# Kernel tuning notes

Measured on AMD Instinct MI355X. Metric: run time of the kernel, lower is better.

## Reference

```python
import jax, jax.numpy as jnp
import numpy as np
from jax import lax

N_LAYER = 4
D_MODEL = 512
N_HEAD = 8
D_HEAD = 64
D_INNER = 2048
KERNEL = 9
POOL = 8
N_CLASSES = 10
BATCH = 4
RAW_LEN = 8192


def setup_inputs() -> dict:
    key = jax.random.key(0)
    ks = jax.random.split(key, 12)
    s = 0.02
    return {
        "signal": jax.random.normal(ks[0], (BATCH, RAW_LEN), jnp.float32),
        "conv_w": jax.random.normal(ks[1], (KERNEL, 1, D_MODEL), jnp.float32) * s,
        "conv_b": jnp.zeros((D_MODEL,), jnp.float32),
        "qkv_w": jax.random.normal(ks[2], (N_LAYER, D_MODEL, 3 * N_HEAD * D_HEAD), jnp.float32) * s,
        "r_w": jax.random.normal(ks[3], (N_LAYER, D_MODEL, N_HEAD * D_HEAD), jnp.float32) * s,
        "o_w": jax.random.normal(ks[4], (N_LAYER, N_HEAD * D_HEAD, D_MODEL), jnp.float32) * s,
        "ff1_w": jax.random.normal(ks[5], (N_LAYER, D_MODEL, D_INNER), jnp.float32) * s,
        "ff1_b": jnp.zeros((N_LAYER, D_INNER), jnp.float32),
        "ff2_w": jax.random.normal(ks[6], (N_LAYER, D_INNER, D_MODEL), jnp.float32) * s,
        "ff2_b": jnp.zeros((N_LAYER, D_MODEL), jnp.float32),
        "r_w_bias": jax.random.normal(ks[7], (N_HEAD, D_HEAD), jnp.float32) * s,
        "r_r_bias": jax.random.normal(ks[8], (N_HEAD, D_HEAD), jnp.float32) * s,
        "fc_w": jax.random.normal(ks[9], (D_MODEL, N_CLASSES), jnp.float32) * s,
        "fc_b": jnp.zeros((N_CLASSES,), jnp.float32),
    }


def _rel_shift(x):
    # x: [qlen, rlen, bsz, n_head]; TF-XL pad/reshape/slice trick
    q, r, b, n = x.shape
    x = jnp.pad(x, ((0, 0), (1, 0), (0, 0), (0, 0)))
    x = x.reshape(r + 1, q, b, n)[1:]
    return x.reshape(q, r, b, n)


def _forward(signal, conv_w, conv_b, qkv_w, r_w, o_w, ff1_w, ff1_b, ff2_w,
             ff2_b, r_w_bias, r_r_bias, fc_w, fc_b):
    # Conv1D (valid) -> ReLU -> AveragePooling1D
    x = signal[:, :, None]  # [B, L, 1]
    x = lax.conv_general_dilated(x, conv_w, (1,), 'VALID',
                                 dimension_numbers=('NWC', 'WIO', 'NWC')) + conv_b
    x = jax.nn.relu(x)
    B, Lp, D = x.shape
    S = Lp // POOL  # Lp is divisible by POOL for our sizes (keras valid pooling)
    x = x[:, :S * POOL].reshape(B, S, POOL, D).mean(axis=2)
    core = x.transpose(1, 0, 2)  # [S, B, D]

    # sinusoidal relative positional embedding, pos_seq = S-1 .. -(S-1)
    pos_seq = jnp.arange(S - 1, -S, -1, dtype=core.dtype)  # [2S-1]
    inv_freq = 1.0 / (10000.0 ** (jnp.arange(0, D, 2, dtype=core.dtype) / D))
    sin_inp = pos_seq[:, None] * inv_freq[None, :]
    pos_emb = jnp.concatenate([jnp.sin(sin_inp), jnp.cos(sin_inp)], -1)  # [2S-1, D]

    scale = 1.0 / np.sqrt(D_HEAD).astype(np.float32)
    for l in range(N_LAYER):
        heads = core @ qkv_w[l]  # [S, B, 3*H*Dh]
        q, k, v = jnp.split(heads, 3, axis=-1)
        q = q.reshape(S, B, N_HEAD, D_HEAD)
        k = k.reshape(S, B, N_HEAD, D_HEAD)
        v = v.reshape(S, B, N_HEAD, D_HEAD)
        rk = (pos_emb @ r_w[l]).reshape(2 * S - 1, N_HEAD, D_HEAD)

        AC = jnp.einsum('ibnd,jbnd->ijbn', q + r_w_bias, k)      # content term
        BD = jnp.einsum('ibnd,jnd->ijbn', q + r_r_bias, rk)      # position term
        BD = _rel_shift(BD)[:, :S]                                # [S, S, B, H]
        attn_prob = jax.nn.softmax((AC + BD) * scale, axis=1)
        attn_vec = jnp.einsum('ijbn,jbnd->ibnd', attn_prob, v)
        attn_out = attn_vec.reshape(S, B, N_HEAD * D_HEAD) @ o_w[l]
        core = core + attn_out

        # position-wise FF with residual
        h = jax.nn.relu(core @ ff1_w[l] + ff1_b[l]) @ ff2_w[l] + ff2_b[l]
        core = core + h

    # classification head on last timestep
    return core[-1] @ fc_w + fc_b  # [B, n_classes]


def reference(signal, conv_w, conv_b, qkv_w, r_w, o_w, ff1_w, ff1_b, ff2_w,
              ff2_b, r_w_bias, r_r_bias, fc_w, fc_b):
    return _forward(signal, conv_w, conv_b, qkv_w, r_w, o_w, ff1_w, ff1_b,
                    ff2_w, ff2_b, r_w_bias, r_r_bias, fc_w, fc_b)
```

## Files before the change

kernel.cpp:

```cpp
#include <hip/hip_runtime.h>
#include <math.h>

#define S_LEN   1023
#define BATCH_N 4
#define DMODEL  512
#define NHEAD   8
#define DHEAD   64
#define DINNER  2048
#define NLAYER  4
#define RAWLEN  8192
#define POOLW   8
#define KERNW   9
#define RLEN    (2*S_LEN-1)
#define MROWS   (S_LEN*BATCH_N)

using bf16x8 = __attribute__((ext_vector_type(8))) short;
using f32x4  = __attribute__((ext_vector_type(4))) float;

__device__ __forceinline__ unsigned short f2bf(float f) {
    union { float f; unsigned int u; } v; v.f = f;
    unsigned int u = v.u;
    return (unsigned short)((u + 0x7fffu + ((u >> 16) & 1u)) >> 16);
}
__device__ __forceinline__ float bf2f(unsigned short h) {
    union { unsigned int u; float f; } v; v.u = ((unsigned int)h) << 16;
    return v.f;
}

__device__ __forceinline__ void gload_lds16(const void* g, void* l) {
    using gvoid = const __attribute__((address_space(1))) void;
    using lvoid = __attribute__((address_space(3))) void;
    gvoid* gp = reinterpret_cast<gvoid*>(reinterpret_cast<unsigned long long>(g));
    lvoid* lp = reinterpret_cast<lvoid*>((unsigned int)reinterpret_cast<unsigned long long>(l));
    __builtin_amdgcn_global_load_lds(gp, lp, 16, 0, 0);
}

__global__ __launch_bounds__(512) void conv_pool_kernel(
    const float* __restrict__ sig, const float* __restrict__ cw,
    const float* __restrict__ cb, float* __restrict__ core,
    unsigned short* __restrict__ core_bf)
{
    int s = blockIdx.x, b = blockIdx.y, d = threadIdx.x;
    __shared__ float sseg[POOLW + KERNW - 1];
    if (d < POOLW + KERNW - 1) sseg[d] = sig[b*RAWLEN + s*POOLW + d];
    __syncthreads();
    float w[KERNW];
#pragma unroll
    for (int k = 0; k < KERNW; k++) w[k] = cw[k*DMODEL + d];
    float bias = cb[d];
    float acc = 0.f;
#pragma unroll
    for (int p = 0; p < POOLW; p++) {
        float c = bias;
#pragma unroll
        for (int k = 0; k < KERNW; k++) c = fmaf(sseg[p+k], w[k], c);
        acc += fmaxf(c, 0.f);
    }
    float v = acc * (1.0f/POOLW);
    core[(s*BATCH_N + b)*DMODEL + d] = v;
    core_bf[(s*BATCH_N + b)*DMODEL + d] = f2bf(v);
}

__global__ __launch_bounds__(512) void posemb_kernel(unsigned short* __restrict__ pe)
{
    int j = blockIdx.x, d = threadIdx.x;
    float pos = (float)(S_LEN - 1 - j);
    int i = (d < 256) ? d : d - 256;
    float invf = exp2f(-(float)i * (13.287712f/256.0f));
    float a = pos * invf;
    pe[j*DMODEL + d] = f2bf((d < 256) ? __sinf(a) : __cosf(a));
}

__global__ __launch_bounds__(256) void transpose_all_kernel(
    const float* __restrict__ qw, const float* __restrict__ rw,
    const float* __restrict__ ow, const float* __restrict__ f1,
    const float* __restrict__ f2,
    unsigned short* __restrict__ qT, unsigned short* __restrict__ rT,
    unsigned short* __restrict__ oT, unsigned short* __restrict__ f1T,
    unsigned short* __restrict__ f2T)
{
    int id = blockIdx.x;
    const float* W; unsigned short* Wt; int K, N, bx, by;
    if (id < 768)       { W = qw;  Wt = qT;  K = 512;  N = 1536; bx = id % 48; by = id / 48; }
    else if (id < 1024) { id -= 768;  W = rw;  Wt = rT;  K = 512;  N = 512;  bx = id % 16; by = id / 16; }
    else if (id < 1280) { id -= 1024; W = ow;  Wt = oT;  K = 512;  N = 512;  bx = id % 16; by = id / 16; }
    else if (id < 2304) { id -= 1280; W = f1;  Wt = f1T; K = 512;  N = 2048; bx = id % 64; by = id / 64; }
    else                { id -= 2304; W = f2;  Wt = f2T; K = 2048; N = 512;  bx = id % 16; by = id / 16; }

    __shared__ float L[32][33];
    int n0 = bx*32, k0 = by*32;
    int t = threadIdx.x;
    int kk = t>>3, nq = (t&7)*4;
    float4 v = *reinterpret_cast<const float4*>(&W[(size_t)(k0+kk)*N + n0 + nq]);
    L[kk][nq+0]=v.x; L[kk][nq+1]=v.y; L[kk][nq+2]=v.z; L[kk][nq+3]=v.w;
    __syncthreads();
    int nn = t>>3, kq = (t&7)*4;
    ushort4 o;
    o.x = f2bf(L[kq+0][nn]); o.y = f2bf(L[kq+1][nn]);
    o.z = f2bf(L[kq+2][nn]); o.w = f2bf(L[kq+3][nn]);
    *reinterpret_cast<ushort4*>(&Wt[(size_t)(n0+nn)*K + k0 + kq]) = o;
}

__global__ __launch_bounds__(256) void vtrans_kernel(
    const unsigned short* __restrict__ heads, unsigned short* __restrict__ vt)
{
    int j0 = blockIdx.x * 64;
    int bn = blockIdx.y; int b = bn >> 3, n = bn & 7;
    __shared__ unsigned short Ls[64*68];
    int t = threadIdx.x;
#pragma unroll
    for (int p = 0; p < 2; p++) {
        int jr = (t>>3) + p*32, sl = (t&7)*8;
        int gj = j0 + jr; if (gj > S_LEN-1) gj = S_LEN-1;
        const unsigned short* src = heads + (size_t)(gj*BATCH_N + b)*1536 + 1024 + n*64 + sl;
        ushort4 a = *reinterpret_cast<const ushort4*>(src);
        ushort4 c = *reinterpret_cast<const ushort4*>(src+4);
        *reinterpret_cast<ushort4*>(&Ls[jr*68 + sl])   = a;
        *reinterpret_cast<ushort4*>(&Ls[jr*68 + sl+4]) = c;
    }
    __syncthreads();
#pragma unroll
    for (int p = 0; p < 2; p++) {
        int d = (t>>3) + p*32, jq = (t&7)*8;
        ushort4 o0, o1;
        o0.x = Ls[(jq+0)*68 + d]; o0.y = Ls[(jq+1)*68 + d];
        o0.z = Ls[(jq+2)*68 + d]; o0.w = Ls[(jq+3)*68 + d];
        o1.x = Ls[(jq+4)*68 + d]; o1.y = Ls[(jq+5)*68 + d];
        o1.z = Ls[(jq+6)*68 + d]; o1.w = Ls[(jq+7)*68 + d];
        unsigned short* dst = vt + ((size_t)bn*64 + d)*1024 + j0 + jq;
        *reinterpret_cast<ushort4*>(dst) = o0;
        *reinterpret_cast<ushort4*>(dst+4) = o1;
    }
}

template<int BN, bool ACCUM, bool BIAS, bool RELU, bool WF32, bool WBF>
__device__ __forceinline__ void gemm_body(
    const unsigned short* __restrict__ A, const unsigned short* __restrict__ Bt,
    const float* __restrict__ bias, float* __restrict__ C,
    unsigned short* __restrict__ Cb, int M, int N, int K, int bm, int bn,
    unsigned short* As, unsigned short* Bs)
{
    constexpr int MF = (BN == 128) ? 4 : 2;
    int tid = threadIdx.x, lane = tid & 63, wid = tid >> 6;

    f32x4 acc[MF][4];
#pragma unroll
    for (int m=0;m<MF;m++)
#pragma unroll
        for (int n=0;n<4;n++) acc[m][n] = (f32x4){0.f,0.f,0.f,0.f};

    int r0 = wid*16 + (lane>>2);
    int slot = (lane&3)*8;
    int ga0 = bm + r0;      if (ga0 > M-1) ga0 = M-1;
    int ga1 = bm + r0 + 64; if (ga1 > M-1) ga1 = M-1;
    const unsigned short* pA0 = A  + (size_t)ga0*K + slot;
    const unsigned short* pA1 = A  + (size_t)ga1*K + slot;
    const unsigned short* pB0 = Bt + (size_t)(bn + r0)*K + slot;
    const unsigned short* pB1 = (BN==128) ? Bt + (size_t)(bn + r0 + 64)*K + slot : nullptr;
    char* lA0 = (char*)As + wid*1024;
    char* lA1 = (char*)As + (wid+4)*1024;
    char* lB0 = (char*)Bs + wid*1024;
    char* lB1 = (char*)Bs + (wid+4)*1024;

    int ar = (BN==128 ? (wid>>1)*64 : wid*32) + (lane&15);
    int br = (BN==128 ? (wid&1)*64 : 0) + (lane&15);
    int kc = (lane>>4)*8;

    for (int k0 = 0; k0 < K; k0 += 32) {
        __syncthreads();
        gload_lds16(pA0, lA0);
        gload_lds16(pA1, lA1);
        gload_lds16(pB0, lB0);
        if (BN == 128) gload_lds16(pB1, lB1);
        pA0 += 32; pA1 += 32; pB0 += 32; if (BN==128) pB1 += 32;
        __syncthreads();
        bf16x8 a[MF], b[4];
#pragma unroll
        for (int m=0;m<MF;m++) a[m] = *reinterpret_cast<const bf16x8*>(&As[(ar + m*16)*32 + kc]);
#pragma unroll
        for (int n=0;n<4;n++) b[n] = *reinterpret_cast<const bf16x8*>(&Bs[(br + n*16)*32 + kc]);
#pragma unroll
        for (int m=0;m<MF;m++)
#pragma unroll
            for (int n=0;n<4;n++)
                acc[m][n] = __builtin_amdgcn_mfma_f32_16x16x32_bf16(a[m], b[n], acc[m][n], 0,0,0);
    }

    int col0 = bn + (BN==128 ? (wid&1)*64 : 0) + (lane&15);
    int rbase = bm + (BN==128 ? (wid>>1)*64 : wid*32) + (lane>>4)*4;
#pragma unroll
    for (int m=0;m<MF;m++) {
#pragma unroll
        for (int n=0;n<4;n++) {
            int col = col0 + n*16;
            float bv = BIAS ? bias[col] : 0.f;
#pragma unroll
            for (int r=0;r<4;r++) {
                int row = rbase + m*16 + r;
                if (row < M) {
                    float v = acc[m][n][r] + bv;
                    if (RELU) v = fmaxf(v, 0.f);
                    size_t off = (size_t)row*N + col;
                    if (ACCUM) v += C[off];
                    if (WF32) C[off] = v;
                    if (WBF)  Cb[off] = f2bf(v);
                }
            }
        }
    }
}

template<int BN, bool ACCUM, bool BIAS, bool RELU, bool WF32, bool WBF>
__global__ __launch_bounds__(256) void gemm_mfma(
    const unsigned short* __restrict__ A, const unsigned short* __restrict__ Bt,
    const float* __restrict__ bias, float* __restrict__ C,
    unsigned short* __restrict__ Cb, int M, int N, int K)
{
    __shared__ unsigned short As[128*32];
    __shared__ unsigned short Bs[BN*32];
    gemm_body<BN,ACCUM,BIAS,RELU,WF32,WBF>(A, Bt, bias, C, Cb, M, N, K,
        blockIdx.y*128, blockIdx.x*BN, As, Bs);
}

__global__ __launch_bounds__(256) void gemm_qkvrk_kernel(
    const unsigned short* __restrict__ core_bf, const unsigned short* __restrict__ qkvT,
    unsigned short* __restrict__ heads,
    const unsigned short* __restrict__ pe_bf, const unsigned short* __restrict__ rwT,
    unsigned short* __restrict__ rk_bf)
{
    __shared__ unsigned short As[128*32];
    __shared__ unsigned short Bs[64*32];
    if (blockIdx.x < 24) {
        gemm_body<64,false,false,false,false,true>(core_bf, qkvT, nullptr, nullptr, heads,
            MROWS, 3*DMODEL, DMODEL, blockIdx.y*128, blockIdx.x*64, As, Bs);
    } else {
        if (blockIdx.y >= 16) return;
        gemm_body<64,false,false,false,false,true>(pe_bf, rwT, nullptr, nullptr, rk_bf,
            RLEN, DMODEL, DMODEL, blockIdx.y*128, (blockIdx.x-24)*64, As, Bs);
    }
}

template<bool ACCUM, bool BIAS, bool RELU, bool WF32, bool WBF>
__global__ __launch_bounds__(256) void gemm_mfma64(
    const unsigned short* __restrict__ A, const unsigned short* __restrict__ Bt,
    const float* __restrict__ bias, float* __restrict__ C,
    unsigned short* __restrict__ Cb, int M, int N, int K)
{
    __shared__ unsigned short As[64*32];
    __shared__ unsigned short Bs[64*32];
    int bm = blockIdx.y * 64, bn = blockIdx.x * 64;
    int tid = threadIdx.x, lane = tid & 63, wid = tid >> 6;
    int wr = wid >> 1, wc = wid & 1;

    f32x4 acc[2][2];
#pragma unroll
    for (int m=0;m<2;m++)
#pragma unroll
        for (int n=0;n<2;n++) acc[m][n] = (f32x4){0.f,0.f,0.f,0.f};

    int r0 = wid*16 + (lane>>2);
    int slot = (lane&3)*8;
    int ga = bm + r0; if (ga > M-1) ga = M-1;
    const unsigned short* pA = A  + (size_t)ga*K + slot;
    const unsigned short* pB = Bt + (size_t)(bn + r0)*K + slot;
    char* lA = (char*)As + wid*1024;
    char* lB = (char*)Bs + wid*1024;

    int ar = wr*32 + (lane&15);
    int br = wc*32 + (lane&15);
    int kc = (lane>>4)*8;

    for (int k0 = 0; k0 < K; k0 += 32) {
        __syncthreads();
        gload_lds16(pA, lA);
        gload_lds16(pB, lB);
        pA += 32; pB += 32;
        __syncthreads();
        bf16x8 a[2], b[2];
#pragma unroll
        for (int m=0;m<2;m++) a[m] = *reinterpret_cast<const bf16x8*>(&As[(ar + m*16)*32 + kc]);
#pragma unroll
        for (int n=0;n<2;n++) b[n] = *reinterpret_cast<const bf16x8*>(&Bs[(br + n*16)*32 + kc]);
#pragma unroll
        for (int m=0;m<2;m++)
#pragma unroll
            for (int n=0;n<2;n++)
                acc[m][n] = __builtin_amdgcn_mfma_f32_16x16x32_bf16(a[m], b[n], acc[m][n], 0,0,0);
    }

    int col0 = bn + wc*32 + (lane&15);
    int rbase = bm + wr*32 + (lane>>4)*4;
#pragma unroll
    for (int m=0;m<2;m++) {
#pragma unroll
        for (int n=0;n<2;n++) {
            int col = col0 + n*16;
            float bv = BIAS ? bias[col] : 0.f;
#pragma unroll
            for (int r=0;r<4;r++) {
                int row = rbase + m*16 + r;
                if (row < M) {
                    float v = acc[m][n][r] + bv;
                    if (RELU) v = fmaxf(v, 0.f);
                    size_t off = (size_t)row*N + col;
                    if (ACCUM) v += C[off];
                    if (WF32) C[off] = v;
                    if (WBF)  Cb[off] = f2bf(v);
                }
            }
        }
    }
}

#define TI 32
#define TJ 32
#define PSTR 40
#define ACSTR 36
#define BDSTR 68

__global__ __launch_bounds__(256) void attn_mfma_kernel(
    const unsigned short* __restrict__ heads,
    const unsigned short* __restrict__ rk,
    const unsigned short* __restrict__ vt,
    const float* __restrict__ rwb, const float* __restrict__ rrb,
    unsigned short* __restrict__ av)
{
    int i0 = blockIdx.x * TI;
    int bn = blockIdx.y; int b = bn >> 3, n = bn & 7;
    int tid = threadIdx.x, lane = tid & 63, wid = tid >> 6;
    int mi = wid >> 1;
    int half = wid & 1;
    int kc = (lane>>4)*8;
    int l15 = lane & 15;

    __shared__ float Sac[TI*ACSTR];
    __shared__ float Sbd[TI*BDSTR];
    __shared__ unsigned short Pb[TI*PSTR];
    __shared__ float mrow[TI], lrow[TI], frow[TI];

    const int base0 = (S_LEN-1) - i0 - (TI-1);

    bf16x8 qwf0, qwf1, qrf0, qrf1;
    {
        int gi = i0 + mi*16 + l15; if (gi > S_LEN-1) gi = S_LEN-1;
        const unsigned short* qb = heads + (size_t)(gi*BATCH_N + b)*1536 + n*64;
        bf16x8 u0 = *reinterpret_cast<const bf16x8*>(qb + kc);
        bf16x8 u1 = *reinterpret_cast<const bf16x8*>(qb + 32 + kc);
#pragma unroll
        for (int e=0;e<8;e++) {
            float f0 = bf2f((unsigned short)u0[e]);
            float f1 = bf2f((unsigned short)u1[e]);
            qwf0[e] = (short)f2bf(f0 + rwb[n*64 + kc + e]);
            qrf0[e] = (short)f2bf(f0 + rrb[n*64 + kc + e]);
            qwf1[e] = (short)f2bf(f1 + rwb[n*64 + 32 + kc + e]);
            qrf1[e] = (short)f2bf(f1 + rrb[n*64 + 32 + kc + e]);
        }
    }
    if (tid < TI) { mrow[tid] = -1e30f; lrow[tid] = 0.f; }

    f32x4 Oa[2];
    Oa[0] = (f32x4){0.f,0.f,0.f,0.f};
    Oa[1] = (f32x4){0.f,0.f,0.f,0.f};

    int rw = mi*16 + (lane>>4)*4;
    const unsigned short* vrow = vt + (size_t)bn*64*1024;

    for (int t = 0; t < 32; t++) {
        int j0 = t * TJ;
        __syncthreads();

        {
            int gj = j0 + half*16 + l15; if (gj > S_LEN-1) gj = S_LEN-1;
            const unsigned short* kb = heads + (size_t)(gj*BATCH_N + b)*1536 + 512 + n*64;
            bf16x8 kf0 = *reinterpret_cast<const bf16x8*>(kb + kc);
            bf16x8 kf1 = *reinterpret_cast<const bf16x8*>(kb + 32 + kc);
            f32x4 s = (f32x4){0.f,0.f,0.f,0.f};
            s = __builtin_amdgcn_mfma_f32_16x16x32_bf16(qwf0, kf0, s, 0,0,0);
            s = __builtin_amdgcn_mfma_f32_16x16x32_bf16(qwf1, kf1, s, 0,0,0);
            int ci = half*16 + l15;
#pragma unroll
            for (int r=0;r<4;r++) Sac[(rw+r)*ACSTR + ci] = s[r];
        }
        if (t == 0) {
#pragma unroll
            for (int nn=0;nn<2;nn++) {
                int w = (half*2+nn)*16 + l15;
                int gr = base0 + w; gr = gr < 0 ? 0 : (gr > RLEN-1 ? RLEN-1 : gr);
                const unsigned short* rb = rk + (size_t)gr*DMODEL + n*64;
                bf16x8 rf0 = *reinterpret_cast<const bf16x8*>(rb + kc);
                bf16x8 rf1 = *reinterpret_cast<const bf16x8*>(rb + 32 + kc);
                f32x4 sb = (f32x4){0.f,0.f,0.f,0.f};
                sb = __builtin_amdgcn_mfma_f32_16x16x32_bf16(qrf0, rf0, sb, 0,0,0);
                sb = __builtin_amdgcn_mfma_f32_16x16x32_bf16(qrf1, rf1, sb, 0,0,0);
#pragma unroll
                for (int r=0;r<4;r++) Sbd[(rw+r)*BDSTR + w] = sb[r];
            }
        } else {
            int pblk = ((t & 1) ? 0 : 2) + half;
            int w = pblk*16 + l15;
            int off = 32*(t+1) + (w & 31);
            int gr = base0 + off; gr = gr < 0 ? 0 : (gr > RLEN-1 ? RLEN-1 : gr);
            const unsigned short* rb = rk + (size_t)gr*DMODEL + n*64;
            bf16x8 rf0 = *reinterpret_cast<const bf16x8*>(rb + kc);
            bf16x8 rf1 = *reinterpret_cast<const bf16x8*>(rb + 32 + kc);
            f32x4 sb = (f32x4){0.f,0.f,0.f,0.f};
            sb = __builtin_amdgcn_mfma_f32_16x16x32_bf16(qrf0, rf0, sb, 0,0,0);
            sb = __builtin_amdgcn_mfma_f32_16x16x32_bf16(qrf1, rf1, sb, 0,0,0);
#pragma unroll
            for (int r=0;r<4;r++) Sbd[(rw+r)*BDSTR + w] = sb[r];
        }
        __syncthreads();

        {
            int r = tid>>3, seg = tid&7, jl = seg*4;
            float4 ac = *reinterpret_cast<const float4*>(&Sac[r*ACSTR + jl]);
            int cbase = 32*t + (TI-1) - r;
            float s0 = (ac.x + Sbd[r*BDSTR + ((cbase+jl+0)&63)]) * 0.125f;
            float s1 = (ac.y + Sbd[r*BDSTR + ((cbase+jl+1)&63)]) * 0.125f;
            float s2 = (ac.z + Sbd[r*BDSTR + ((cbase+jl+2)&63)]) * 0.125f;
            float s3 = (ac.w + Sbd[r*BDSTR + ((cbase+jl+3)&63)]) * 0.125f;
            int jg = j0 + jl;
            if (jg+0 >= S_LEN) s0 = -1e30f;
            if (jg+1 >= S_LEN) s1 = -1e30f;
            if (jg+2 >= S_LEN) s2 = -1e30f;
            if (jg+3 >= S_LEN) s3 = -1e30f;
            float tm = fmaxf(fmaxf(s0,s1), fmaxf(s2,s3));
            tm = fmaxf(tm, __shfl_xor(tm, 1));
            tm = fmaxf(tm, __shfl_xor(tm, 2));
            tm = fmaxf(tm, __shfl_xor(tm, 4));
            float mo = mrow[r];
            float mnew = fmaxf(mo, tm);
            float f = __expf(mo - mnew);
            float e0 = __expf(s0 - mnew), e1 = __expf(s1 - mnew);
            float e2 = __expf(s2 - mnew), e3 = __expf(s3 - mnew);
            float ssum = e0+e1+e2+e3;
            ssum += __shfl_xor(ssum, 1);
            ssum += __shfl_xor(ssum, 2);
            ssum += __shfl_xor(ssum, 4);
            if (seg == 0) {
                mrow[r] = mnew;
                lrow[r] = lrow[r]*f + ssum;
                frow[r] = f;
            }
            ushort4 pw;
            pw.x = f2bf(e0); pw.y = f2bf(e1); pw.z = f2bf(e2); pw.w = f2bf(e3);
            *reinterpret_cast<ushort4*>(&Pb[r*PSTR + jl]) = pw;
        }
        __syncthreads();

        {
            float f0 = frow[rw+0], f1 = frow[rw+1], f2 = frow[rw+2], f3 = frow[rw+3];
#pragma unroll
            for (int nn=0;nn<2;nn++) {
                Oa[nn][0] *= f0; Oa[nn][1] *= f1; Oa[nn][2] *= f2; Oa[nn][3] *= f3;
            }
            bf16x8 pf = *reinterpret_cast<const bf16x8*>(&Pb[(mi*16 + l15)*PSTR + kc]);
#pragma unroll
            for (int nn=0;nn<2;nn++) {
                int d = (half*2+nn)*16 + l15;
                bf16x8 vf = *reinterpret_cast<const bf16x8*>(&vrow[(size_t)d*1024 + j0 + kc]);
                Oa[nn] = __builtin_amdgcn_mfma_f32_16x16x32_bf16(pf, vf, Oa[nn], 0,0,0);
            }
        }
    }
    __syncthreads();

    {
        float linv[4];
#pragma unroll
        for (int r=0;r<4;r++) linv[r] = 1.0f / lrow[rw+r];
#pragma unroll
        for (int nn=0;nn<2;nn++) {
            int d = (half*2+nn)*16 + l15;
#pragma unroll
            for (int r=0;r<4;r++) {
                int gi = i0 + rw + r;
                if (gi < S_LEN)
                    av[(size_t)(gi*BATCH_N + b)*DMODEL + n*64 + d] = f2bf(Oa[nn][r]*linv[r]);
            }
        }
    }
}

__global__ __launch_bounds__(64) void final_kernel(
    const float* __restrict__ core, const float* __restrict__ fcw,
    const float* __restrict__ fcb, float* __restrict__ out)
{
    int idx = blockIdx.x;
    int b = idx / 10, c = idx % 10;
    int lane = threadIdx.x;
    const float* row = &core[(size_t)((S_LEN-1)*BATCH_N + b)*DMODEL];
    float acc = 0.f;
    for (int d = lane; d < DMODEL; d += 64)
        acc = fmaf(row[d], fcw[d*10 + c], acc);
#pragma unroll
    for (int off = 32; off; off >>= 1) acc += __shfl_xor(acc, off);
    if (lane == 0) out[b*10 + c] = acc + fcb[c];
}

extern "C" void kernel_launch(void* const* d_in, const int* in_sizes, int n_in,
                              void* d_out, int out_size, void* d_ws, size_t ws_size,
                              hipStream_t stream)
{
    const float* sig   = (const float*)d_in[0];
    const float* cw    = (const float*)d_in[1];
    const float* cb    = (const float*)d_in[2];
    const float* qkv_w = (const float*)d_in[3];
    const float* r_w   = (const float*)d_in[4];
    const float* o_w   = (const float*)d_in[5];
    const float* ff1_w = (const float*)d_in[6];
    const float* ff1_b = (const float*)d_in[7];
    const float* ff2_w = (const float*)d_in[8];
    const float* ff2_b = (const float*)d_in[9];
    const float* rwb   = (const float*)d_in[10];
    const float* rrb   = (const float*)d_in[11];
    const float* fcw   = (const float*)d_in[12];
    const float* fcb   = (const float*)d_in[13];
    float* out = (float*)d_out;

    float* core = (float*)d_ws;
    unsigned short* core_bf = (unsigned short*)(core + (size_t)MROWS*DMODEL);
    unsigned short* pe_bf   = core_bf + (size_t)MROWS*DMODEL;
    unsigned short* rk_bf   = pe_bf   + (size_t)RLEN*DMODEL;
    unsigned short* av_bf   = rk_bf   + (size_t)RLEN*DMODEL;
    unsigned short* big_bf  = av_bf   + (size_t)MROWS*DMODEL;
    unsigned short* qkvT = big_bf + (size_t)MROWS*DINNER;
    unsigned short* rwT  = qkvT + (size_t)(3*DMODEL)*DMODEL;
    unsigned short* owT  = rwT  + (size_t)DMODEL*DMODEL;
    unsigned short* ff1T = owT  + (size_t)DMODEL*DMODEL;
    unsigned short* ff2T = ff1T + (size_t)DINNER*DMODEL;
    unsigned short* vt   = ff2T + (size_t)DMODEL*DINNER;

    conv_pool_kernel<<<dim3(S_LEN, BATCH_N), 512, 0, stream>>>(sig, cw, cb, core, core_bf);
    posemb_kernel<<<RLEN, 512, 0, stream>>>(pe_bf);

    for (int l = 0; l < NLAYER; l++) {
        transpose_all_kernel<<<3328, 256, 0, stream>>>(
            qkv_w + (size_t)l*DMODEL*(3*DMODEL),
            r_w   + (size_t)l*DMODEL*DMODEL,
            o_w   + (size_t)l*DMODEL*DMODEL,
            ff1_w + (size_t)l*DMODEL*DINNER,
            ff2_w + (size_t)l*DINNER*DMODEL,
            qkvT, rwT, owT, ff1T, ff2T);

        gemm_qkvrk_kernel<<<dim3(32,32), 256, 0, stream>>>(
            core_bf, qkvT, big_bf, pe_bf, rwT, rk_bf);
        vtrans_kernel<<<dim3(16,32), 256, 0, stream>>>(big_bf, vt);
        attn_mfma_kernel<<<dim3(32,32), 256, 0, stream>>>(big_bf, rk_bf, vt, rwb, rrb, av_bf);
        gemm_mfma64<true,false,false,true,true><<<dim3(8,64), 256, 0, stream>>>(
            av_bf, owT, nullptr, core, core_bf, MROWS, DMODEL, DMODEL);
        gemm_mfma<128,false,true,true,false,true><<<dim3(16,32), 256, 0, stream>>>(
            core_bf, ff1T, ff1_b + (size_t)l*DINNER, nullptr, big_bf, MROWS, DINNER, DMODEL);
        gemm_mfma64<true,true,false,true,true><<<dim3(8,64), 256, 0, stream>>>(
            big_bf, ff2T, ff2_b + (size_t)l*DMODEL, core, core_bf, MROWS, DMODEL, DINNER);
    }

    final_kernel<<<40, 64, 0, stream>>>(core, fcw, fcb, out);
}
```

Before: 753.0 us.

## Drop V transpose kernel and prefetch K/R fragments across attention iterations

Removes the separate vtrans kernel and instead gathers V fragments inside the attention kernel with scalar strided 16-bit loads straight from the qkv buffer. K and positional-key fragments for the next tile are now loaded one iteration ahead into registers, so their latency overlaps the current softmax work. This saves one kernel launch and a global round trip per layer. In exchange, the V loads become uncoalesced 2-byte accesses per element, and register pressure rises.

```diff
diff --git a/kernel.cpp b/kernel.cpp
--- a/kernel.cpp
+++ b/kernel.cpp
@@ -101,38 +101,6 @@
     *reinterpret_cast<ushort4*>(&Wt[(size_t)(n0+nn)*K + k0 + kq]) = o;
 }
 
-__global__ __launch_bounds__(256) void vtrans_kernel(
-    const unsigned short* __restrict__ heads, unsigned short* __restrict__ vt)
-{
-    int j0 = blockIdx.x * 64;
-    int bn = blockIdx.y; int b = bn >> 3, n = bn & 7;
-    __shared__ unsigned short Ls[64*68];
-    int t = threadIdx.x;
-#pragma unroll
-    for (int p = 0; p < 2; p++) {
-        int jr = (t>>3) + p*32, sl = (t&7)*8;
-        int gj = j0 + jr; if (gj > S_LEN-1) gj = S_LEN-1;
-        const unsigned short* src = heads + (size_t)(gj*BATCH_N + b)*1536 + 1024 + n*64 + sl;
-        ushort4 a = *reinterpret_cast<const ushort4*>(src);
-        ushort4 c = *reinterpret_cast<const ushort4*>(src+4);
-        *reinterpret_cast<ushort4*>(&Ls[jr*68 + sl])   = a;
-        *reinterpret_cast<ushort4*>(&Ls[jr*68 + sl+4]) = c;
-    }
-    __syncthreads();
-#pragma unroll
-    for (int p = 0; p < 2; p++) {
-        int d = (t>>3) + p*32, jq = (t&7)*8;
-        ushort4 o0, o1;
-        o0.x = Ls[(jq+0)*68 + d]; o0.y = Ls[(jq+1)*68 + d];
-        o0.z = Ls[(jq+2)*68 + d]; o0.w = Ls[(jq+3)*68 + d];
-        o1.x = Ls[(jq+4)*68 + d]; o1.y = Ls[(jq+5)*68 + d];
-        o1.z = Ls[(jq+6)*68 + d]; o1.w = Ls[(jq+7)*68 + d];
-        unsigned short* dst = vt + ((size_t)bn*64 + d)*1024 + j0 + jq;
-        *reinterpret_cast<ushort4*>(dst) = o0;
-        *reinterpret_cast<ushort4*>(dst+4) = o1;
-    }
-}
-
 template<int BN, bool ACCUM, bool BIAS, bool RELU, bool WF32, bool WBF>
 __device__ __forceinline__ void gemm_body(
     const unsigned short* __restrict__ A, const unsigned short* __restrict__ Bt,
@@ -321,7 +289,6 @@
 __global__ __launch_bounds__(256) void attn_mfma_kernel(
     const unsigned short* __restrict__ heads,
     const unsigned short* __restrict__ rk,
-    const unsigned short* __restrict__ vt,
     const float* __restrict__ rwb, const float* __restrict__ rrb,
     unsigned short* __restrict__ av)
 {
@@ -363,17 +330,32 @@
     Oa[1] = (f32x4){0.f,0.f,0.f,0.f};
 
     int rw = mi*16 + (lane>>4)*4;
-    const unsigned short* vrow = vt + (size_t)bn*64*1024;
+
+    bf16x8 kf0, kf1, rA0, rA1, rB0, rB1;
+    {
+        int gj = half*16 + l15; if (gj > S_LEN-1) gj = S_LEN-1;
+        const unsigned short* kb = heads + (size_t)(gj*BATCH_N + b)*1536 + 512 + n*64;
+        kf0 = *reinterpret_cast<const bf16x8*>(kb + kc);
+        kf1 = *reinterpret_cast<const bf16x8*>(kb + 32 + kc);
+    }
+    {
+        int w = (half*2+0)*16 + l15;
+        int gr = base0 + w; gr = gr < 0 ? 0 : (gr > RLEN-1 ? RLEN-1 : gr);
+        const unsigned short* rb = rk + (size_t)gr*DMODEL + n*64;
+        rA0 = *reinterpret_cast<const bf16x8*>(rb + kc);
+        rA1 = *reinterpret_cast<const bf16x8*>(rb + 32 + kc);
+        w = (half*2+1)*16 + l15;
+        gr = base0 + w; gr = gr < 0 ? 0 : (gr > RLEN-1 ? RLEN-1 : gr);
+        rb = rk + (size_t)gr*DMODEL + n*64;
+        rB0 = *reinterpret_cast<const bf16x8*>(rb + kc);
+        rB1 = *reinterpret_cast<const bf16x8*>(rb + 32 + kc);
+    }
 
     for (int t = 0; t < 32; t++) {
         int j0 = t * TJ;
         __syncthreads();
 
         {
-            int gj = j0 + half*16 + l15; if (gj > S_LEN-1) gj = S_LEN-1;
-            const unsigned short* kb = heads + (size_t)(gj*BATCH_N + b)*1536 + 512 + n*64;
-            bf16x8 kf0 = *reinterpret_cast<const bf16x8*>(kb + kc);
-            bf16x8 kf1 = *reinterpret_cast<const bf16x8*>(kb + 32 + kc);
             f32x4 s = (f32x4){0.f,0.f,0.f,0.f};
             s = __builtin_amdgcn_mfma_f32_16x16x32_bf16(qwf0, kf0, s, 0,0,0);
             s = __builtin_amdgcn_mfma_f32_16x16x32_bf16(qwf1, kf1, s, 0,0,0);
@@ -382,32 +364,52 @@
             for (int r=0;r<4;r++) Sac[(rw+r)*ACSTR + ci] = s[r];
         }
         if (t == 0) {
-#pragma unroll
-            for (int nn=0;nn<2;nn++) {
-                int w = (half*2+nn)*16 + l15;
-                int gr = base0 + w; gr = gr < 0 ? 0 : (gr > RLEN-1 ? RLEN-1 : gr);
-                const unsigned short* rb = rk + (size_t)gr*DMODEL + n*64;
-                bf16x8 rf0 = *reinterpret_cast<const bf16x8*>(rb + kc);
-                bf16x8 rf1 = *reinterpret_cast<const bf16x8*>(rb + 32 + kc);
-                f32x4 sb = (f32x4){0.f,0.f,0.f,0.f};
-                sb = __builtin_amdgcn_mfma_f32_16x16x32_bf16(qrf0, rf0, sb, 0,0,0);
-                sb = __builtin_amdgcn_mfma_f32_16x16x32_bf16(qrf1, rf1, sb, 0,0,0);
-#pragma unroll
-                for (int r=0;r<4;r++) Sbd[(rw+r)*BDSTR + w] = sb[r];
-            }
+            f32x4 sb = (f32x4){0.f,0.f,0.f,0.f};
+            sb = __builtin_amdgcn_mfma_f32_16x16x32_bf16(qrf0, rA0, sb, 0,0,0);
+            sb = __builtin_amdgcn_mfma_f32_16x16x32_bf16(qrf1, rA1, sb, 0,0,0);
+            int w = (half*2+0)*16 + l15;
+#pragma unroll
+            for (int r=0;r<4;r++) Sbd[(rw+r)*BDSTR + w] = sb[r];
+            sb = (f32x4){0.f,0.f,0.f,0.f};
+            sb = __builtin_amdgcn_mfma_f32_16x16x32_bf16(qrf0, rB0, sb, 0,0,0);
+            sb = __builtin_amdgcn_mfma_f32_16x16x32_bf16(qrf1, rB1, sb, 0,0,0);
+            w = (half*2+1)*16 + l15;
+#pragma unroll
+            for (int r=0;r<4;r++) Sbd[(rw+r)*BDSTR + w] = sb[r];
         } else {
             int pblk = ((t & 1) ? 0 : 2) + half;
             int w = pblk*16 + l15;
-            int off = 32*(t+1) + (w & 31);
-            int gr = base0 + off; gr = gr < 0 ? 0 : (gr > RLEN-1 ? RLEN-1 : gr);
+            f32x4 sb = (f32x4){0.f,0.f,0.f,0.f};
+            sb = __builtin_amdgcn_mfma_f32_16x16x32_bf16(qrf0, rA0, sb, 0,0,0);
+            sb = __builtin_amdgcn_mfma_f32_16x16x32_bf16(qrf1, rA1, sb, 0,0,0);
+#pragma unroll
+            for (int r=0;r<4;r++) Sbd[(rw+r)*BDSTR + w] = sb[r];
+        }
+        if (t < 31) {
+            int gj = (t+1)*TJ + half*16 + l15; if (gj > S_LEN-1) gj = S_LEN-1;
+            const unsigned short* kb = heads + (size_t)(gj*BATCH_N + b)*1536 + 512 + n*64;
+            kf0 = *reinterpret_cast<const bf16x8*>(kb + kc);
+            kf1 = *reinterpret_cast<const bf16x8*>(kb + 32 + kc);
+            int pblkN = (((t+1) & 1) ? 0 : 2) + half;
+            int wN = pblkN*16 + l15;
+            int offN = 32*(t+2) + (wN & 31);
+            int gr = base0 + offN; gr = gr < 0 ? 0 : (gr > RLEN-1 ? RLEN-1 : gr);
             const unsigned short* rb = rk + (size_t)gr*DMODEL + n*64;
-            bf16x8 rf0 = *reinterpret_cast<const bf16x8*>(rb + kc);
-            bf16x8 rf1 = *reinterpret_cast<const bf16x8*>(rb + 32 + kc);
-            f32x4 sb = (f32x4){0.f,0.f,0.f,0.f};
-            sb = __builtin_amdgcn_mfma_f32_16x16x32_bf16(qrf0, rf0, sb, 0,0,0);
-            sb = __builtin_amdgcn_mfma_f32_16x16x32_bf16(qrf1, rf1, sb, 0,0,0);
-#pragma unroll
-            for (int r=0;r<4;r++) Sbd[(rw+r)*BDSTR + w] = sb[r];
+            rA0 = *reinterpret_cast<const bf16x8*>(rb + kc);
+            rA1 = *reinterpret_cast<const bf16x8*>(rb + 32 + kc);
+        }
+        bf16x8 vf0, vf1;
+        {
+            const unsigned short* vb = heads + 1024 + n*64;
+            int d0 = (half*2+0)*16 + l15;
+            int d1 = (half*2+1)*16 + l15;
+#pragma unroll
+            for (int e=0;e<8;e++) {
+                int gj = j0 + kc + e; if (gj > S_LEN-1) gj = S_LEN-1;
+                size_t rowb = (size_t)(gj*BATCH_N + b)*1536;
+                vf0[e] = (short)vb[rowb + d0];
+                vf1[e] = (short)vb[rowb + d1];
+            }
         }
         __syncthreads();
 
@@ -450,17 +452,11 @@
 
         {
             float f0 = frow[rw+0], f1 = frow[rw+1], f2 = frow[rw+2], f3 = frow[rw+3];
-#pragma unroll
-            for (int nn=0;nn<2;nn++) {
-                Oa[nn][0] *= f0; Oa[nn][1] *= f1; Oa[nn][2] *= f2; Oa[nn][3] *= f3;
-            }
+            Oa[0][0] *= f0; Oa[0][1] *= f1; Oa[0][2] *= f2; Oa[0][3] *= f3;
+            Oa[1][0] *= f0; Oa[1][1] *= f1; Oa[1][2] *= f2; Oa[1][3] *= f3;
             bf16x8 pf = *reinterpret_cast<const bf16x8*>(&Pb[(mi*16 + l15)*PSTR + kc]);
-#pragma unroll
-            for (int nn=0;nn<2;nn++) {
-                int d = (half*2+nn)*16 + l15;
-                bf16x8 vf = *reinterpret_cast<const bf16x8*>(&vrow[(size_t)d*1024 + j0 + kc]);
-                Oa[nn] = __builtin_amdgcn_mfma_f32_16x16x32_bf16(pf, vf, Oa[nn], 0,0,0);
-            }
+            Oa[0] = __builtin_amdgcn_mfma_f32_16x16x32_bf16(pf, vf0, Oa[0], 0,0,0);
+            Oa[1] = __builtin_amdgcn_mfma_f32_16x16x32_bf16(pf, vf1, Oa[1], 0,0,0);
         }
     }
     __syncthreads();
@@ -476,7 +472,8 @@
             for (int r=0;r<4;r++) {
                 int gi = i0 + rw + r;
                 if (gi < S_LEN)
-                    av[(size_t)(gi*BATCH_N + b)*DMODEL + n*64 + d] = f2bf(Oa[nn][r]*linv[r]);
+                    av[(size_t)(gi*BATCH_N + b)*DMODEL + n*64 + d] =
+                        f2bf((nn == 0 ? Oa[0][r] : Oa[1][r]) * linv[r]);
             }
         }
     }
@@ -529,7 +526,6 @@
     unsigned short* owT  = rwT  + (size_t)DMODEL*DMODEL;
     unsigned short* ff1T = owT  + (size_t)DMODEL*DMODEL;
     unsigned short* ff2T = ff1T + (size_t)DINNER*DMODEL;
-    unsigned short* vt   = ff2T + (size_t)DMODEL*DINNER;
 
     conv_pool_kernel<<<dim3(S_LEN, BATCH_N), 512, 0, stream>>>(sig, cw, cb, core, core_bf);
     posemb_kernel<<<RLEN, 512, 0, stream>>>(pe_bf);
@@ -545,8 +541,7 @@
 
         gemm_qkvrk_kernel<<<dim3(32,32), 256, 0, stream>>>(
             core_bf, qkvT, big_bf, pe_bf, rwT, rk_bf);
-        vtrans_kernel<<<dim3(16,32), 256, 0, stream>>>(big_bf, vt);
-        attn_mfma_kernel<<<dim3(32,32), 256, 0, stream>>>(big_bf, rk_bf, vt, rwb, rrb, av_bf);
+        attn_mfma_kernel<<<dim3(32,32), 256, 0, stream>>>(big_bf, rk_bf, rwb, rrb, av_bf);
         gemm_mfma64<true,false,false,true,true><<<dim3(8,64), 256, 0, stream>>>(
             av_bf, owT, nullptr, core, core_bf, MROWS, DMODEL, DMODEL);
         gemm_mfma<128,false,true,true,false,true><<<dim3(16,32), 256, 0, stream>>>(
```

Result: faster. 715.2 us (-5.0%).
